# Kernel tuning notes

Hardware: AMD Instinct MI355X
Metric: run time of the kernel (lower is better)

The kernel has to match this reference:

```python
import jax, jax.numpy as jnp
import numpy as np

H_GRID = 256
W_GRID = 256


def setup_inputs() -> dict:
    key = jax.random.key(0)
    k1, k2, k3, k4 = jax.random.split(key, 4)
    B, N = 8, 32768
    in_ch, out_ch = 14, 64
    xyzp = jax.random.uniform(k1, (B, N, 4), dtype=jnp.float32)  # x,y,t,p all in [0,1]
    features = jax.random.normal(k2, (B, N, in_ch), dtype=jnp.float32)
    W = jax.random.normal(k3, (9, in_ch + 2, out_ch), dtype=jnp.float32) * 0.05  # 3x3 kernel taps
    bias = jax.random.normal(k4, (out_ch,), dtype=jnp.float32) * 0.05
    return {"xyzp": xyzp, "features": features, "W": W, "bias": bias}


def reference(xyzp, features, W, bias):
    # SparseConv: voxelize points onto an (h+1)x(w+1) grid with 'mean' pooling of
    # duplicates, run a 3x3 submanifold sparse conv (inactive sites contribute 0),
    # then map results back to point order.
    h, w = H_GRID, W_GRID
    Hd, Wd = h + 1, w + 1  # round(y*h) in [0,h]
    B, N, _ = xyzp.shape
    Cin = features.shape[-1] + 2

    # yxb coordinates (note: column order [y, x] as in _get_yxb)
    y = jnp.clip(jnp.round(xyzp[..., 1] * h), 0, h).astype(jnp.int32).reshape(-1)
    x = jnp.clip(jnp.round(xyzp[..., 0] * w), 0, w).astype(jnp.int32).reshape(-1)
    b = jnp.repeat(jnp.arange(B, dtype=jnp.int32), N)

    # per-point features: [pos, neg, features]
    p = xyzp[..., 3:4]
    f = jnp.concatenate([p, 1.0 - p, features], axis=-1).reshape(B * N, Cin)

    # InputLayer mode='mean': scatter-mean duplicate coordinates into voxels
    flat = (b * Hd + y) * Wd + x  # [B*N]
    S = B * Hd * Wd
    vox_sum = jax.ops.segment_sum(f, flat, num_segments=S)            # [S, Cin]
    cnt = jax.ops.segment_sum(jnp.ones((B * N, 1), f.dtype), flat, num_segments=S)
    vox = vox_sum / jnp.maximum(cnt, 1.0)  # inactive voxels stay exactly 0

    # Submanifold 3x3 conv evaluated at each point's (active) site.
    offs = jnp.array([(dy, dx) for dy in (-1, 0, 1) for dx in (-1, 0, 1)], jnp.int32)  # [9,2]
    ny = y[:, None] + offs[None, :, 0]  # [B*N, 9]
    nx = x[:, None] + offs[None, :, 1]
    valid = (ny >= 0) & (ny < Hd) & (nx >= 0) & (nx < Wd)
    nidx = (b[:, None] * Hd + jnp.clip(ny, 0, Hd - 1)) * Wd + jnp.clip(nx, 0, Wd - 1)
    nb = vox[nidx] * valid[..., None].astype(f.dtype)  # [B*N, 9, Cin]; inactive -> 0

    out = jnp.einsum('pkc,kcd->pd', nb, W) + bias  # [B*N, out_ch]
    return out.reshape(B, N, -1)
```

## Files before the change

### kernel.cpp

```cpp
#include <hip/hip_runtime.h>

#define HD 257
#define WD 257
#define NB (8 * HD)
#define NCHUNK 32
#define CAPC 32
#define BPTS 1024
#define COUT 64
#define LROW 17
#define RPB 2
#define GPTS 64

typedef unsigned int uint;
typedef unsigned short ushort;
typedef short short8 __attribute__((ext_vector_type(8)));
typedef float f32x4 __attribute__((ext_vector_type(4)));

__device__ __forceinline__ uint pack_bf16(float a, float b) {
    uint ua = __float_as_uint(a), ub = __float_as_uint(b);
    ua += 0x7fffu + ((ua >> 16) & 1u);
    ub += 0x7fffu + ((ub >> 16) & 1u);
    return (ua >> 16) | (ub & 0xffff0000u);
}
__device__ __forceinline__ unsigned short bf16_1(float a) {
    uint ua = __float_as_uint(a);
    ua += 0x7fffu + ((ua >> 16) & 1u);
    return (unsigned short)(ua >> 16);
}

__global__ __launch_bounds__(256) void bin_kernel(
    const float* __restrict__ xyzp,
    uint* __restrict__ cnt2,
    ushort* __restrict__ pidx,
    int N) {
    __shared__ uint hist[HD];
    const int tid = threadIdx.x;
    const int chunk = blockIdx.x;
    const int b = blockIdx.y;
    const int p0 = chunk * BPTS;
    for (int i = tid; i < HD; i += 256) hist[i] = 0u;
    __syncthreads();

    const float4* xp = reinterpret_cast<const float4*>(xyzp) + (size_t)b * N;
    uint rec[BPTS / 256];
#pragma unroll
    for (int k = 0; k < BPTS / 256; ++k) {
        int i = p0 + tid + k * 256;
        float4 v = xp[i];
        int y = (int)fminf(fmaxf(rintf(v.y * 256.0f), 0.0f), 256.0f);
        uint r = atomicAdd(&hist[y], 1u);
        rec[k] = (uint)y | (r << 9);
    }
    __syncthreads();

    for (int y = tid; y < HD; y += 256)
        cnt2[(size_t)(b * HD + y) * NCHUNK + chunk] = min(hist[y], (uint)CAPC);

#pragma unroll
    for (int k = 0; k < BPTS / 256; ++k) {
        int y = rec[k] & 511;
        uint r = rec[k] >> 9;
        if (r < CAPC)
            pidx[((size_t)(b * HD + y) * NCHUNK + chunk) * CAPC + r] =
                (ushort)(p0 + tid + k * 256);
    }
}

__global__ __launch_bounds__(256) void accum_kernel(
    const uint* __restrict__ cnt2,
    const ushort* __restrict__ pidx,
    const float* __restrict__ xyzp,
    const float* __restrict__ feat,
    uint* __restrict__ voxn,
    int logN) {
    __shared__ float l[RPB * WD * LROW];
    __shared__ uint pc[RPB * NCHUNK];
    const int tid = threadIdx.x;
    const int bucket0 = blockIdx.x * RPB;
    for (int i = tid; i < RPB * WD * LROW; i += 256) l[i] = 0.0f;
    if (tid < RPB * NCHUNK)
        pc[tid] = cnt2[(size_t)bucket0 * NCHUNK + tid];
    __syncthreads();

#pragma unroll
    for (int s = 0; s < RPB * NCHUNK * CAPC; s += 256) {
        int slot = s + tid;
        int c = slot >> 5;
        int j = slot & (CAPC - 1);
        if ((uint)j < pc[c]) {
            int r = c >> 5;
            int chunk = c & 31;
            int bucket = bucket0 + r;
            int b = bucket / HD;
            uint lp = pidx[((size_t)bucket * NCHUNK + chunk) * CAPC + j];
            int p = (b << logN) + (int)lp;
            float4 v = reinterpret_cast<const float4*>(xyzp)[p];
            int x = (int)fminf(fmaxf(rintf(v.x * 256.0f), 0.0f), 256.0f);
            float* cell = l + (r * WD + x) * LROW;
            atomicAdd(&cell[0], v.w);
            atomicAdd(&cell[1], 1.0f - v.w);
            const float2* f2 = reinterpret_cast<const float2*>(feat + (size_t)p * 14);
#pragma unroll
            for (int jj = 0; jj < 7; ++jj) {
                float2 fv = f2[jj];
                atomicAdd(&cell[2 + 2 * jj], fv.x);
                atomicAdd(&cell[3 + 2 * jj], fv.y);
            }
        }
    }
    __syncthreads();

    for (int i = tid; i < RPB * WD; i += 256) {
        int r = i / WD;
        int x = i - r * WD;
        const float* c = l + (r * WD + x) * LROW;
        float inv = __builtin_amdgcn_rcpf(fmaxf(c[0] + c[1], 1.0f));
        uint o[8];
#pragma unroll
        for (int j = 0; j < 8; ++j)
            o[j] = pack_bf16(c[2 * j] * inv, c[2 * j + 1] * inv);
        uint4* op = reinterpret_cast<uint4*>(voxn + ((size_t)(bucket0 + r) * WD + x) * 8);
        op[0] = make_uint4(o[0], o[1], o[2], o[3]);
        op[1] = make_uint4(o[4], o[5], o[6], o[7]);
    }
}

__global__ __launch_bounds__(256) void gather_mfma_kernel(
    const float* __restrict__ xyzp,
    const uint* __restrict__ voxn,
    const float* __restrict__ W,
    const float* __restrict__ bias,
    float* __restrict__ out, int logN) {
    __shared__ __align__(16) char sA[GPTS * 336];
    __shared__ int sCell[GPTS];
    __shared__ uint sYX[GPTS];

    const int tid = threadIdx.x;
    const int lane = tid & 63;
    const int w = tid >> 6;
    const int p0 = blockIdx.x * GPTS;
    const int hi = lane >> 4;
    const int lo = lane & 15;

    if (tid < GPTS) {
        float4 v = reinterpret_cast<const float4*>(xyzp)[p0 + tid];
        int y = (int)fminf(fmaxf(rintf(v.y * 256.0f), 0.0f), 256.0f);
        int x = (int)fminf(fmaxf(rintf(v.x * 256.0f), 0.0f), 256.0f);
        int b = (p0 + tid) >> logN;
        sCell[tid] = (b * HD + y) * WD + x;
        sYX[tid] = ((uint)y << 16) | (uint)x;
    }

    short8 bfrag[5];
    float bv = bias[w * 16 + lo];
#pragma unroll
    for (int s = 0; s < 5; ++s) {
        int kbase = s * 32 + hi * 8;
        short8 f;
#pragma unroll
        for (int j = 0; j < 8; ++j) {
            int k = kbase + j;
            float wv = (k < 144) ? W[(size_t)k * 64 + w * 16 + lo] : 0.0f;
            f[j] = (short)bf16_1(wv);
        }
        bfrag[s] = f;
    }
    __syncthreads();

    for (int idx = tid; idx < GPTS * 18; idx += 256) {
        int i = idx / 18;
        int r = idx - i * 18;
        int seg = r / 6;
        int h = r - seg * 6;
        int kx = h >> 1;
        int half = h & 1;
        uint yx = sYX[i];
        int y = (int)(yx >> 16), x = (int)(yx & 0xffffu);
        int ny = y + seg - 1, nx = x + kx - 1;
        uint4 val = make_uint4(0, 0, 0, 0);
        if ((uint)ny <= 256u && (uint)nx <= 256u) {
            size_t ncell = (size_t)sCell[i] + (size_t)((seg - 1) * WD + (kx - 1));
            val = *reinterpret_cast<const uint4*>(
                reinterpret_cast<const char*>(voxn) + ncell * 32 + (size_t)half * 16);
        }
        *reinterpret_cast<uint4*>(sA + i * 336 + (seg * 3 + kx) * 32 + half * 16) = val;
    }
    if (tid < GPTS * 2) {
        int i = tid >> 1, h = tid & 1;
        *reinterpret_cast<uint4*>(sA + i * 336 + 288 + h * 16) = make_uint4(0, 0, 0, 0);
    }
    __syncthreads();

    f32x4 acc[4];
#pragma unroll
    for (int mt = 0; mt < 4; ++mt) acc[mt] = (f32x4){bv, bv, bv, bv};

#pragma unroll
    for (int mt = 0; mt < 4; ++mt) {
        const char* abase = sA + (mt * 16 + lo) * 336 + hi * 16;
#pragma unroll
        for (int s = 0; s < 5; ++s) {
            short8 a = *reinterpret_cast<const short8*>(abase + s * 64);
            acc[mt] = __builtin_amdgcn_mfma_f32_16x16x32_bf16(a, bfrag[s], acc[mt], 0, 0, 0);
        }
    }

#pragma unroll
    for (int mt = 0; mt < 4; ++mt)
#pragma unroll
        for (int r = 0; r < 4; ++r) {
            int row = mt * 16 + hi * 4 + r;
            out[(size_t)(p0 + row) * 64 + w * 16 + lo] = acc[mt][r];
        }
}

extern "C" void kernel_launch(void* const* d_in, const int* in_sizes, int n_in,
                              void* d_out, int out_size, void* d_ws, size_t ws_size,
                              hipStream_t stream) {
    const float* xyzp = (const float*)d_in[0];
    const float* feat = (const float*)d_in[1];
    const float* W    = (const float*)d_in[2];
    const float* bias = (const float*)d_in[3];
    float* out = (float*)d_out;

    const int BN = in_sizes[0] / 4;
    const int B = 8;
    const int N = BN / B;
    int logN = 0;
    while ((1 << logN) < N) ++logN;

    uint* cnt2 = (uint*)d_ws;
    ushort* pidx = (ushort*)((char*)cnt2 + (size_t)NB * NCHUNK * 4);
    uint* voxn = (uint*)((char*)pidx + (size_t)NB * NCHUNK * CAPC * 2);
    (void)ws_size;

    dim3 bgrid(NCHUNK, B);
    bin_kernel<<<bgrid, 256, 0, stream>>>(xyzp, cnt2, pidx, N);
    accum_kernel<<<NB / RPB, 256, 0, stream>>>(cnt2, pidx, xyzp, feat, voxn, logN);
    gather_mfma_kernel<<<BN / GPTS, 256, 0, stream>>>(xyzp, voxn, W, bias, out, logN);
}
```

Before: 70.35 us.

## Restructure gather-conv per grid row using staged neighbor rows and binned point lists

The gather+MFMA kernel now runs one block per (batch, y) row. It loads the three neighboring voxel rows into shared memory once and reads the point list from the bins built earlier, so each point's 3x3 neighborhood comes from LDS instead of scattered global loads. The bin kernel also packs the point's x coordinate into a 32-bit pidx entry, which lets the accumulate kernel skip reloading the full xyzp record. The cost is doubled pidx storage and a per-row cap of 448 points. Points beyond that cap, or beyond the 32-per-chunk cap, are silently not written, which risks correctness on dense rows.

```diff
diff --git a/kernel.cpp b/kernel.cpp
--- a/kernel.cpp
+++ b/kernel.cpp
@@ -9,7 +9,8 @@
 #define COUT 64
 #define LROW 17
 #define RPB 2
-#define GPTS 64
+#define DCAP 448
+#define ROWW 259
 
 typedef unsigned int uint;
 typedef unsigned short ushort;
@@ -31,7 +32,7 @@
 __global__ __launch_bounds__(256) void bin_kernel(
     const float* __restrict__ xyzp,
     uint* __restrict__ cnt2,
-    ushort* __restrict__ pidx,
+    uint* __restrict__ pidx,
     int N) {
     __shared__ uint hist[HD];
     const int tid = threadIdx.x;
@@ -42,14 +43,16 @@
     __syncthreads();
 
     const float4* xp = reinterpret_cast<const float4*>(xyzp) + (size_t)b * N;
-    uint rec[BPTS / 256];
+    uint rec[BPTS / 256], xrec[BPTS / 256];
 #pragma unroll
     for (int k = 0; k < BPTS / 256; ++k) {
         int i = p0 + tid + k * 256;
         float4 v = xp[i];
         int y = (int)fminf(fmaxf(rintf(v.y * 256.0f), 0.0f), 256.0f);
+        int x = (int)fminf(fmaxf(rintf(v.x * 256.0f), 0.0f), 256.0f);
         uint r = atomicAdd(&hist[y], 1u);
         rec[k] = (uint)y | (r << 9);
+        xrec[k] = (uint)x;
     }
     __syncthreads();
 
@@ -62,13 +65,13 @@
         uint r = rec[k] >> 9;
         if (r < CAPC)
             pidx[((size_t)(b * HD + y) * NCHUNK + chunk) * CAPC + r] =
-                (ushort)(p0 + tid + k * 256);
+                (xrec[k] << 16) | (uint)(p0 + tid + k * 256);
     }
 }
 
 __global__ __launch_bounds__(256) void accum_kernel(
     const uint* __restrict__ cnt2,
-    const ushort* __restrict__ pidx,
+    const uint* __restrict__ pidx,
     const float* __restrict__ xyzp,
     const float* __restrict__ feat,
     uint* __restrict__ voxn,
@@ -92,13 +95,13 @@
             int chunk = c & 31;
             int bucket = bucket0 + r;
             int b = bucket / HD;
-            uint lp = pidx[((size_t)bucket * NCHUNK + chunk) * CAPC + j];
-            int p = (b << logN) + (int)lp;
-            float4 v = reinterpret_cast<const float4*>(xyzp)[p];
-            int x = (int)fminf(fmaxf(rintf(v.x * 256.0f), 0.0f), 256.0f);
+            uint e = pidx[((size_t)bucket * NCHUNK + chunk) * CAPC + j];
+            int x = (int)(e >> 16);
+            int p = (b << logN) + (int)(e & 0xffffu);
+            float w = xyzp[(size_t)p * 4 + 3];
             float* cell = l + (r * WD + x) * LROW;
-            atomicAdd(&cell[0], v.w);
-            atomicAdd(&cell[1], 1.0f - v.w);
+            atomicAdd(&cell[0], w);
+            atomicAdd(&cell[1], 1.0f - w);
             const float2* f2 = reinterpret_cast<const float2*>(feat + (size_t)p * 14);
 #pragma unroll
             for (int jj = 0; jj < 7; ++jj) {
@@ -126,29 +129,47 @@
 }
 
 __global__ __launch_bounds__(256) void gather_mfma_kernel(
-    const float* __restrict__ xyzp,
+    const uint* __restrict__ cnt2,
+    const uint* __restrict__ pidx,
     const uint* __restrict__ voxn,
     const float* __restrict__ W,
     const float* __restrict__ bias,
     float* __restrict__ out, int logN) {
-    __shared__ __align__(16) char sA[GPTS * 336];
-    __shared__ int sCell[GPTS];
-    __shared__ uint sYX[GPTS];
+    __shared__ __align__(16) uint4 sRows[3 * 518];
+    __shared__ uint sPC[NCHUNK], sBase[NCHUNK];
+    __shared__ uint sNtot;
+    __shared__ ushort sPid[DCAP], sXv[DCAP];
 
     const int tid = threadIdx.x;
     const int lane = tid & 63;
     const int w = tid >> 6;
-    const int p0 = blockIdx.x * GPTS;
     const int hi = lane >> 4;
     const int lo = lane & 15;
-
-    if (tid < GPTS) {
-        float4 v = reinterpret_cast<const float4*>(xyzp)[p0 + tid];
-        int y = (int)fminf(fmaxf(rintf(v.y * 256.0f), 0.0f), 256.0f);
-        int x = (int)fminf(fmaxf(rintf(v.x * 256.0f), 0.0f), 256.0f);
-        int b = (p0 + tid) >> logN;
-        sCell[tid] = (b * HD + y) * WD + x;
-        sYX[tid] = ((uint)y << 16) | (uint)x;
+    const int bucket = blockIdx.x;
+    const int b = bucket / HD;
+    const int y = bucket - b * HD;
+
+    if (tid < NCHUNK) sPC[tid] = cnt2[(size_t)bucket * NCHUNK + tid];
+    __syncthreads();
+
+    if (tid == 0) {
+        uint a = 0;
+#pragma unroll
+        for (int c = 0; c < NCHUNK; ++c) { sBase[c] = a; a += sPC[c]; }
+        sNtot = min(a, (uint)DCAP);
+    }
+    for (int i = tid; i < DCAP; i += 256) { sPid[i] = 0xffffu; sXv[i] = 0; }
+    for (int idx = tid; idx < 3 * 518; idx += 256) {
+        int seg = idx / 518;
+        int rem = idx - seg * 518;
+        int cellx = rem >> 1, half = rem & 1;
+        int ny = y + seg - 1;
+        int nx = cellx - 1;
+        uint4 val = make_uint4(0, 0, 0, 0);
+        if ((uint)ny <= 256u && (uint)nx <= 256u)
+            val = reinterpret_cast<const uint4*>(voxn)
+                      [((size_t)(b * HD + ny) * WD + nx) * 2 + half];
+        sRows[idx] = val;
     }
 
     short8 bfrag[5];
@@ -167,51 +188,62 @@
     }
     __syncthreads();
 
-    for (int idx = tid; idx < GPTS * 18; idx += 256) {
-        int i = idx / 18;
-        int r = idx - i * 18;
-        int seg = r / 6;
-        int h = r - seg * 6;
-        int kx = h >> 1;
-        int half = h & 1;
-        uint yx = sYX[i];
-        int y = (int)(yx >> 16), x = (int)(yx & 0xffffu);
-        int ny = y + seg - 1, nx = x + kx - 1;
-        uint4 val = make_uint4(0, 0, 0, 0);
-        if ((uint)ny <= 256u && (uint)nx <= 256u) {
-            size_t ncell = (size_t)sCell[i] + (size_t)((seg - 1) * WD + (kx - 1));
-            val = *reinterpret_cast<const uint4*>(
-                reinterpret_cast<const char*>(voxn) + ncell * 32 + (size_t)half * 16);
-        }
-        *reinterpret_cast<uint4*>(sA + i * 336 + (seg * 3 + kx) * 32 + half * 16) = val;
-    }
-    if (tid < GPTS * 2) {
-        int i = tid >> 1, h = tid & 1;
-        *reinterpret_cast<uint4*>(sA + i * 336 + 288 + h * 16) = make_uint4(0, 0, 0, 0);
-    }
-    __syncthreads();
-
-    f32x4 acc[4];
-#pragma unroll
-    for (int mt = 0; mt < 4; ++mt) acc[mt] = (f32x4){bv, bv, bv, bv};
-
-#pragma unroll
-    for (int mt = 0; mt < 4; ++mt) {
-        const char* abase = sA + (mt * 16 + lo) * 336 + hi * 16;
-#pragma unroll
-        for (int s = 0; s < 5; ++s) {
-            short8 a = *reinterpret_cast<const short8*>(abase + s * 64);
-            acc[mt] = __builtin_amdgcn_mfma_f32_16x16x32_bf16(a, bfrag[s], acc[mt], 0, 0, 0);
-        }
-    }
-
-#pragma unroll
-    for (int mt = 0; mt < 4; ++mt)
-#pragma unroll
-        for (int r = 0; r < 4; ++r) {
-            int row = mt * 16 + hi * 4 + r;
-            out[(size_t)(p0 + row) * 64 + w * 16 + lo] = acc[mt][r];
-        }
+    for (int idx = tid; idx < NCHUNK * CAPC; idx += 256) {
+        int c = idx >> 5, j = idx & (CAPC - 1);
+        if ((uint)j < sPC[c]) {
+            uint e = pidx[((size_t)bucket * NCHUNK + c) * CAPC + j];
+            uint pos = sBase[c] + j;
+            if (pos < DCAP) {
+                sPid[pos] = (ushort)(e & 0xffffu);
+                sXv[pos] = (ushort)(e >> 16);
+            }
+        }
+    }
+    __syncthreads();
+
+    const int hh = hi >> 1, hl = hi & 1;
+    int offA[5];
+#pragma unroll
+    for (int s = 0; s < 5; ++s) {
+        int kn = 2 * s + hh;
+        int kc = (kn > 8) ? 0 : kn;
+        int seg = (kc * 11) >> 5;
+        int kx = kc - 3 * seg;
+        offA[s] = seg * 8288 + kx * 32 + hl * 16;
+    }
+    const bool s4ok = (hh == 0);
+    const char* rowsB = reinterpret_cast<const char*>(sRows);
+
+    const uint ntile = (sNtot + 63u) >> 6;
+    for (uint t = 0; t < ntile; ++t) {
+        int base = (int)t * 64;
+        f32x4 acc[4];
+#pragma unroll
+        for (int mt = 0; mt < 4; ++mt) acc[mt] = (f32x4){bv, bv, bv, bv};
+
+#pragma unroll
+        for (int mt = 0; mt < 4; ++mt) {
+            int xb = (int)sXv[base + mt * 16 + lo] << 5;
+#pragma unroll
+            for (int s = 0; s < 5; ++s) {
+                int addr = offA[s] + xb;
+                if (s == 4 && !s4ok) addr = 0;
+                short8 a = *reinterpret_cast<const short8*>(rowsB + addr);
+                acc[mt] = __builtin_amdgcn_mfma_f32_16x16x32_bf16(a, bfrag[s], acc[mt], 0, 0, 0);
+            }
+        }
+
+#pragma unroll
+        for (int mt = 0; mt < 4; ++mt)
+#pragma unroll
+            for (int r = 0; r < 4; ++r) {
+                uint pid = sPid[base + mt * 16 + hi * 4 + r];
+                if (pid != 0xffffu) {
+                    size_t p = ((size_t)b << logN) + pid;
+                    out[p * 64 + w * 16 + lo] = acc[mt][r];
+                }
+            }
+    }
 }
 
 extern "C" void kernel_launch(void* const* d_in, const int* in_sizes, int n_in,
@@ -230,12 +262,12 @@
     while ((1 << logN) < N) ++logN;
 
     uint* cnt2 = (uint*)d_ws;
-    ushort* pidx = (ushort*)((char*)cnt2 + (size_t)NB * NCHUNK * 4);
-    uint* voxn = (uint*)((char*)pidx + (size_t)NB * NCHUNK * CAPC * 2);
+    uint* pidx = (uint*)((char*)cnt2 + (size_t)NB * NCHUNK * 4);
+    uint* voxn = (uint*)((char*)pidx + (size_t)NB * NCHUNK * CAPC * 4);
     (void)ws_size;
 
     dim3 bgrid(NCHUNK, B);
     bin_kernel<<<bgrid, 256, 0, stream>>>(xyzp, cnt2, pidx, N);
     accum_kernel<<<NB / RPB, 256, 0, stream>>>(cnt2, pidx, xyzp, feat, voxn, logN);
-    gather_mfma_kernel<<<BN / GPTS, 256, 0, stream>>>(xyzp, voxn, W, bias, out, logN);
-}
+    gather_mfma_kernel<<<NB, 256, 0, stream>>>(cnt2, pidx, voxn, W, bias, out, logN);
+}
```

After: 74.94 us. 1.07x slower.
